# Optimization experiments

Hardware: AMD Instinct MI355X
Metric: run time of the kernel (lower is better)

Reference implementation:

```python
import jax, jax.numpy as jnp
import numpy as np

N_PEP = 50000
N_PROT = 50000
H = 256
F_IN = 1280
E = 300000
EL = 200000


def setup_inputs() -> dict:
    key = jax.random.key(0)
    ks = jax.random.split(key, 16)
    s = 0.02
    return {
        "x_pep": jax.random.normal(ks[0], (N_PEP, F_IN), jnp.float32),
        "x_prot": jax.random.normal(ks[1], (N_PROT, F_IN), jnp.float32),
        "Wpep": s * jax.random.normal(ks[2], (H, F_IN), jnp.float32),
        "bpep": jnp.zeros((H,), jnp.float32),
        "Wprot": s * jax.random.normal(ks[3], (H, F_IN), jnp.float32),
        "bprot": jnp.zeros((H,), jnp.float32),
        "Wl1": s * jax.random.normal(ks[4], (3, H, H), jnp.float32),
        "bl1": jnp.zeros((3, H), jnp.float32),
        "Wr1": s * jax.random.normal(ks[5], (3, H, H), jnp.float32),
        "Wl2": s * jax.random.normal(ks[6], (3, H, H), jnp.float32),
        "bl2": jnp.zeros((3, H), jnp.float32),
        "Wr2": s * jax.random.normal(ks[7], (3, H, H), jnp.float32),
        "ei_pp": jax.random.randint(ks[8], (2, E), 0, N_PEP, jnp.int32),   # pep -> prot
        "ei_rp": jax.random.randint(ks[9], (2, E), 0, N_PROT, jnp.int32),  # prot -> pep (reverse)
        "ei_prot": jax.random.randint(ks[10], (2, E), 0, N_PROT, jnp.int32),  # prot -> prot
        "eli_het": jax.random.randint(ks[11], (2, EL), 0, N_PEP, jnp.int32),
        "eli_homo": jax.random.randint(ks[12], (2, EL), 0, N_PROT, jnp.int32),
    }


def _seg_mean(src_feat, dst_idx, n_dst):
    # mean aggregation of edge messages into destination nodes
    s = jax.ops.segment_sum(src_feat, dst_idx, num_segments=n_dst)
    cnt = jax.ops.segment_sum(jnp.ones((dst_idx.shape[0], 1), src_feat.dtype), dst_idx, num_segments=n_dst)
    return s / jnp.maximum(cnt, 1.0)


def _sage(x_src, x_dst, ei, Wl, bl, Wr):
    # PyG SAGEConv(aggr='mean'): lin_l(mean_j x_j) + lin_r(x_i); lin_r has no bias
    m = _seg_mean(x_src[ei[0]], ei[1], x_dst.shape[0])
    return m @ Wl.T + bl + x_dst @ Wr.T


def reference(x_pep, x_prot, Wpep, bpep, Wprot, bprot,
              Wl1, bl1, Wr1, Wl2, bl2, Wr2,
              ei_pp, ei_rp, ei_prot, eli_het, eli_homo):
    # feat_src == 'esm': linear projection of ESM features
    h_pep = x_pep @ Wpep.T + bpep
    h_prot = x_prot @ Wprot.T + bprot

    # --- hetero SAGE layer 1 (to_hetero: sum over edge types per dst type) ---
    p1 = jax.nn.relu(_sage(h_prot, h_pep, ei_rp, Wl1[1], bl1[1], Wr1[1]))
    q1 = jax.nn.relu(_sage(h_pep, h_prot, ei_pp, Wl1[0], bl1[0], Wr1[0])
                     + _sage(h_prot, h_prot, ei_prot, Wl1[2], bl1[2], Wr1[2]))

    # --- hetero SAGE layer 2 ---
    p2 = _sage(q1, p1, ei_rp, Wl2[1], bl2[1], Wr2[1])
    q2 = (_sage(p1, q1, ei_pp, Wl2[0], bl2[0], Wr2[0])
          + _sage(q1, q1, ei_prot, Wl2[2], bl2[2], Wr2[2]))

    # edge classifiers: gather + elementwise mul + sum
    het_pred = (p2[eli_het[0]] * q2[eli_het[1]]).sum(axis=-1)
    homo_pred = (q2[eli_homo[0]] * q2[eli_homo[1]]).sum(axis=-1)
    return (het_pred, homo_pred)
```

## Files before the change

### kernel.cpp

```cpp
#include <hip/hip_runtime.h>

using u16 = unsigned short;
using u32 = unsigned int;

#define H 256
#define NNODE 50000
#define CAP 32
#define BM 128
#define BN 128
#define BK 64

typedef __attribute__((ext_vector_type(8))) short bf16x8;
typedef __attribute__((ext_vector_type(4))) float f32x4;

struct AChunks { const void* p[3]; };

__device__ __forceinline__ u16 f2b(float f) {
    u32 u = __builtin_bit_cast(u32, f);
    return (u16)((u + 0x7FFFu + ((u >> 16) & 1u)) >> 16);
}
__device__ __forceinline__ float b2f(u16 h) {
    u32 u = ((u32)h) << 16;
    return __builtin_bit_cast(float, u);
}
__device__ __forceinline__ void gld_lds16(const void* g, void* l) {
    __builtin_amdgcn_global_load_lds(
        (__attribute__((address_space(1))) void*)(void*)g,
        (__attribute__((address_space(3))) void*)l, 16, 0, 0);
}
__device__ __forceinline__ u32 packbf(float a, float b) {
    return (u32)f2b(a) | ((u32)f2b(b) << 16);
}

template<bool AF32, bool RELU>
__global__ __launch_bounds__(512) void gemm_pipe(
    AChunks ac, int aStride, const u16* __restrict__ Bw,
    const float* __restrict__ bias, u16* __restrict__ C, int M, int Ktot)
{
    __shared__ __align__(16) char As[2][BM * 128];
    __shared__ __align__(16) char Bs[2][BN * 128];

    const int tid = threadIdx.x;
    const int l   = tid & 63;
    const int w   = tid >> 6;
    const int wr  = w >> 2, wc = w & 3;
    const int m0  = blockIdx.x * BM;
    const int n0  = blockIdx.y * BN;
    const int nk  = Ktot >> 6;

    f32x4 acc[4][2];
#pragma unroll
    for (int i = 0; i < 4; ++i)
#pragma unroll
        for (int j = 0; j < 2; ++j) acc[i][j] = f32x4{0.f, 0.f, 0.f, 0.f};

    auto stageB = [&](int k, int bi) {
        int k0 = k * 64;
#pragma unroll
        for (int i = 0; i < 2; ++i) {
            int ci = i * 512 + tid;
            int r = ci >> 3, c16 = ci & 7;
            int sb = (c16 * 16) ^ ((r & 7) << 4);
            const u16* g = Bw + (size_t)(n0 + r) * Ktot + k0 + (sb >> 1);
            gld_lds16(g, &Bs[bi][ci * 16]);
        }
    };
    auto stageAb = [&](int k, int bi) {
        int k0 = k * 64;
        const u16* base = (const u16*)ac.p[k0 >> 8];
        int kk = k0 & 255;
#pragma unroll
        for (int i = 0; i < 2; ++i) {
            int ci = i * 512 + tid;
            int r = ci >> 3, c16 = ci & 7;
            int row = m0 + r; row = row < M ? row : M - 1;
            int sb = (c16 * 16) ^ ((r & 7) << 4);
            const u16* g = base + (size_t)row * aStride + kk + (sb >> 1);
            gld_lds16(g, &As[bi][ci * 16]);
        }
    };
    auto loadAf = [&](int k, float4 (&rA)[4]) {
        int k0 = k * 64;
        const float* base = (const float*)ac.p[0];
        int r = tid >> 2;
        int row = m0 + r; row = row < M ? row : M - 1;
        const float* g = base + (size_t)row * aStride + k0 + (tid & 3) * 16;
#pragma unroll
        for (int j = 0; j < 4; ++j) rA[j] = *(const float4*)(g + j * 4);
    };
    auto writeAf = [&](float4 (&rA)[4], int bi) {
        int r  = tid >> 2;
        int cb = (tid & 3) * 32;
        int sw = (r & 7) << 4;
        uint4 lo, hi;
        lo.x = packbf(rA[0].x, rA[0].y); lo.y = packbf(rA[0].z, rA[0].w);
        lo.z = packbf(rA[1].x, rA[1].y); lo.w = packbf(rA[1].z, rA[1].w);
        hi.x = packbf(rA[2].x, rA[2].y); hi.y = packbf(rA[2].z, rA[2].w);
        hi.z = packbf(rA[3].x, rA[3].y); hi.w = packbf(rA[3].z, rA[3].w);
        *(uint4*)&As[bi][r * 128 + (cb ^ sw)]        = lo;
        *(uint4*)&As[bi][r * 128 + ((cb + 16) ^ sw)] = hi;
    };
    auto compute = [&](int bi) {
#pragma unroll
        for (int ks = 0; ks < 2; ++ks) {
            bf16x8 af[4], bfr[2];
#pragma unroll
            for (int mi = 0; mi < 4; ++mi) {
                int r = wr * 64 + mi * 16 + (l & 15);
                int off = (ks * 64 + (l >> 4) * 16) ^ ((r & 7) << 4);
                af[mi] = *(const bf16x8*)&As[bi][r * 128 + off];
            }
#pragma unroll
            for (int ni = 0; ni < 2; ++ni) {
                int r = wc * 32 + ni * 16 + (l & 15);
                int off = (ks * 64 + (l >> 4) * 16) ^ ((r & 7) << 4);
                bfr[ni] = *(const bf16x8*)&Bs[bi][r * 128 + off];
            }
#pragma unroll
            for (int mi = 0; mi < 4; ++mi)
#pragma unroll
                for (int ni = 0; ni < 2; ++ni)
                    acc[mi][ni] = __builtin_amdgcn_mfma_f32_16x16x32_bf16(
                        af[mi], bfr[ni], acc[mi][ni], 0, 0, 0);
        }
    };
    auto body = [&](int k, float4 (&rA)[4], int cur) {
        if (AF32) {
            asm volatile("s_waitcnt vmcnt(6)" ::: "memory");
            writeAf(rA, cur);
            asm volatile("s_waitcnt lgkmcnt(0)" ::: "memory");
        } else {
            asm volatile("s_waitcnt vmcnt(4)" ::: "memory");
        }
        __builtin_amdgcn_sched_barrier(0);
        __builtin_amdgcn_s_barrier();
        __builtin_amdgcn_sched_barrier(0);
        compute(cur);
        __builtin_amdgcn_sched_barrier(0);
        __builtin_amdgcn_s_barrier();
        __builtin_amdgcn_sched_barrier(0);
        int kq = k + 2; if (kq > nk - 1) kq = nk - 1;
        stageB(kq, cur);
        __builtin_amdgcn_sched_barrier(0);
        if (AF32) loadAf(kq, rA);
        else      stageAb(kq, cur);
        __builtin_amdgcn_sched_barrier(0);
    };

    float4 rA0[4], rA1[4];
    if (AF32) {
        stageB(0, 0); __builtin_amdgcn_sched_barrier(0);
        loadAf(0, rA0); __builtin_amdgcn_sched_barrier(0);
        stageB(1, 1); __builtin_amdgcn_sched_barrier(0);
        loadAf(1, rA1); __builtin_amdgcn_sched_barrier(0);
    } else {
        stageB(0, 0); stageAb(0, 0);
        __builtin_amdgcn_sched_barrier(0);
        stageB(1, 1); stageAb(1, 1);
        __builtin_amdgcn_sched_barrier(0);
    }
    for (int k = 0; k < nk; k += 2) {
        body(k,     rA0, 0);
        body(k + 1, rA1, 1);
    }

    const int fr = l & 15, fq = l >> 4;
#pragma unroll
    for (int ni = 0; ni < 2; ++ni) {
        int col = n0 + wc * 32 + ni * 16 + fr;
        float bv = bias ? bias[col] : 0.f;
#pragma unroll
        for (int mi = 0; mi < 4; ++mi) {
            int rowb = m0 + wr * 64 + mi * 16 + fq * 4;
#pragma unroll
            for (int j = 0; j < 4; ++j) {
                int row = rowb + j;
                if (row < M) {
                    float v = acc[mi][ni][j] + bv;
                    if (RELU) v = fmaxf(v, 0.f);
                    C[(size_t)row * H + col] = f2b(v);
                }
            }
        }
    }
}

__global__ __launch_bounds__(256) void fill_zero(float4* __restrict__ p, size_t n4)
{
    size_t i = (size_t)blockIdx.x * blockDim.x + threadIdx.x;
    size_t stride = (size_t)gridDim.x * blockDim.x;
    for (; i < n4; i += stride) p[i] = make_float4(0.f, 0.f, 0.f, 0.f);
}

__global__ __launch_bounds__(256) void build_bucket(
    const int* __restrict__ src, const int* __restrict__ dst, int nE,
    int* __restrict__ cnt, int* __restrict__ bucket)
{
    int i = blockIdx.x * blockDim.x + threadIdx.x;
    if (i >= nE) return;
    int d = dst[i];
    int pos = atomicAdd(&cnt[d], 1);
    if (pos < CAP) bucket[(size_t)d * CAP + pos] = src[i];
}

__global__ __launch_bounds__(256) void seg_mean_gather(
    const u16* __restrict__ feat, const int* __restrict__ bucket,
    const int* __restrict__ cnt, int n_dst, u16* __restrict__ out)
{
    int d = (int)(((size_t)blockIdx.x * blockDim.x + threadIdx.x) >> 6);
    int lane = threadIdx.x & 63;
    if (d >= n_dst) return;
    int c = cnt[d];
    int cc = c < CAP ? c : CAP;
    const int* b = bucket + (size_t)d * CAP;
    float a0 = 0.f, a1 = 0.f, a2 = 0.f, a3 = 0.f;
    int i = 0;
    for (; i + 4 <= cc; i += 4) {
        int s0 = b[i], s1 = b[i + 1], s2 = b[i + 2], s3 = b[i + 3];
        uint2 v0 = *(const uint2*)(feat + (size_t)s0 * H + lane * 4);
        uint2 v1 = *(const uint2*)(feat + (size_t)s1 * H + lane * 4);
        uint2 v2 = *(const uint2*)(feat + (size_t)s2 * H + lane * 4);
        uint2 v3 = *(const uint2*)(feat + (size_t)s3 * H + lane * 4);
        a0 += b2f((u16)(v0.x & 0xffff)) + b2f((u16)(v1.x & 0xffff))
            + b2f((u16)(v2.x & 0xffff)) + b2f((u16)(v3.x & 0xffff));
        a1 += b2f((u16)(v0.x >> 16)) + b2f((u16)(v1.x >> 16))
            + b2f((u16)(v2.x >> 16)) + b2f((u16)(v3.x >> 16));
        a2 += b2f((u16)(v0.y & 0xffff)) + b2f((u16)(v1.y & 0xffff))
            + b2f((u16)(v2.y & 0xffff)) + b2f((u16)(v3.y & 0xffff));
        a3 += b2f((u16)(v0.y >> 16)) + b2f((u16)(v1.y >> 16))
            + b2f((u16)(v2.y >> 16)) + b2f((u16)(v3.y >> 16));
    }
    for (; i < cc; ++i) {
        uint2 v = *(const uint2*)(feat + (size_t)b[i] * H + lane * 4);
        a0 += b2f((u16)(v.x & 0xffff));
        a1 += b2f((u16)(v.x >> 16));
        a2 += b2f((u16)(v.y & 0xffff));
        a3 += b2f((u16)(v.y >> 16));
    }
    float inv = 1.0f / fmaxf((float)c, 1.0f);
    uint2 o;
    o.x = packbf(a0 * inv, a1 * inv);
    o.y = packbf(a2 * inv, a3 * inv);
    *(uint2*)(out + (size_t)d * H + lane * 4) = o;
}

__global__ __launch_bounds__(256) void edge_dot(
    const u16* __restrict__ P, const u16* __restrict__ Q,
    const int* __restrict__ ia, const int* __restrict__ ib,
    int nE, float* __restrict__ out)
{
    int gi = blockIdx.x * 256 + threadIdx.x;
    int e = gi >> 5, l32 = gi & 31;
    if (e >= nE) return;
    uint4 a = *(const uint4*)(P + (size_t)ia[e] * H + l32 * 8);
    uint4 b = *(const uint4*)(Q + (size_t)ib[e] * H + l32 * 8);
    float v = 0.f;
    v += b2f((u16)(a.x & 0xffff)) * b2f((u16)(b.x & 0xffff));
    v += b2f((u16)(a.x >> 16))    * b2f((u16)(b.x >> 16));
    v += b2f((u16)(a.y & 0xffff)) * b2f((u16)(b.y & 0xffff));
    v += b2f((u16)(a.y >> 16))    * b2f((u16)(b.y >> 16));
    v += b2f((u16)(a.z & 0xffff)) * b2f((u16)(b.z & 0xffff));
    v += b2f((u16)(a.z >> 16))    * b2f((u16)(b.z >> 16));
    v += b2f((u16)(a.w & 0xffff)) * b2f((u16)(b.w & 0xffff));
    v += b2f((u16)(a.w >> 16))    * b2f((u16)(b.w >> 16));
#pragma unroll
    for (int off = 16; off; off >>= 1) v += __shfl_xor(v, off);
    if (l32 == 0) out[e] = v;
}

struct PackTab {
    const float* s1[12]; const float* s2[12]; u16* dst[12];
    int Ks[12], Kdst[12], koff[12], blk0[13];
};
__global__ __launch_bounds__(256) void pack_all(PackTab t)
{
    int b = blockIdx.x;
    int it = 0;
    while (it < 11 && b >= t.blk0[it + 1]) ++it;
    int idx = (b - t.blk0[it]) * 1024 + threadIdx.x * 4;
    int Ks = t.Ks[it];
    if (idx >= 256 * Ks) return;
    int n = idx / Ks;
    int k = idx - n * Ks;
    float4 v = *(const float4*)(t.s1[it] + idx);
    if (t.s2[it]) {
        float4 u = *(const float4*)(t.s2[it] + idx);
        v.x += u.x; v.y += u.y; v.z += u.z; v.w += u.w;
    }
    ushort4 h;
    h.x = f2b(v.x); h.y = f2b(v.y); h.z = f2b(v.z); h.w = f2b(v.w);
    *(ushort4*)(t.dst[it] + (size_t)n * t.Kdst[it] + t.koff[it] + k) = h;
}

__global__ void bias_pair(const float* __restrict__ bl1, const float* __restrict__ bl2,
                          float* __restrict__ bq1, float* __restrict__ bq2)
{
    int i = threadIdx.x;
    if (blockIdx.x == 0) bq1[i] = bl1[i] + bl1[512 + i];
    else                 bq2[i] = bl2[i] + bl2[512 + i];
}

static inline void launch_gemm3(const void* a0, const void* a1, const void* a2,
                                const u16* Bw, const float* bias, u16* C,
                                int Ktot, bool relu, hipStream_t s)
{
    AChunks ac = {{a0, a1, a2}};
    dim3 grid((NNODE + BM - 1) / BM, H / BN);
    if (relu) gemm_pipe<false, true><<<grid, 512, 0, s>>>(ac, 256, Bw, bias, C, NNODE, Ktot);
    else      gemm_pipe<false, false><<<grid, 512, 0, s>>>(ac, 256, Bw, bias, C, NNODE, Ktot);
}

extern "C" void kernel_launch(void* const* d_in, const int* in_sizes, int n_in,
                              void* d_out, int out_size, void* d_ws, size_t ws_size,
                              hipStream_t stream)
{
    const float* x_pep  = (const float*)d_in[0];
    const float* x_prot = (const float*)d_in[1];
    const float* Wpep   = (const float*)d_in[2];
    const float* bpep   = (const float*)d_in[3];
    const float* Wprot  = (const float*)d_in[4];
    const float* bprot  = (const float*)d_in[5];
    const float* Wl1    = (const float*)d_in[6];
    const float* bl1    = (const float*)d_in[7];
    const float* Wr1    = (const float*)d_in[8];
    const float* Wl2    = (const float*)d_in[9];
    const float* bl2    = (const float*)d_in[10];
    const float* Wr2    = (const float*)d_in[11];
    const int* ei_pp    = (const int*)d_in[12];
    const int* ei_rp    = (const int*)d_in[13];
    const int* ei_prot  = (const int*)d_in[14];
    const int* eli_het  = (const int*)d_in[15];
    const int* eli_homo = (const int*)d_in[16];

    const int E  = in_sizes[12] / 2;
    const int EL = in_sizes[15] / 2;
    const int FIN = in_sizes[2] / H;

    float* out = (float*)d_out;

    const size_t nodeElems = (size_t)NNODE * H;
    u16* bufA = (u16*)d_ws;
    u16* bufB = bufA + nodeElems;
    u16* bufC = bufB + nodeElems;
    u16* bufD = bufC + nodeElems;
    u16* bufE = bufD + nodeElems;
    u16* bufF = bufE + nodeElems;
    u16* Bpep  = bufF + nodeElems;
    u16* Bprot = Bpep  + (size_t)256 * 1280;
    u16* Bp1   = Bprot + (size_t)256 * 1280;
    u16* Bq1   = Bp1   + (size_t)256 * 512;
    u16* Bp2   = Bq1   + (size_t)256 * 768;
    u16* Bq2   = Bp2   + (size_t)256 * 512;
    float* bq1 = (float*)(Bq2 + (size_t)256 * 768);
    float* bq2 = bq1 + 256;
    int* cntRP   = (int*)(bq2 + 256);
    int* cntPP   = cntRP + NNODE;
    int* cntPR   = cntPP + NNODE;
    int* bktRP   = cntPR + NNODE;
    int* bktPP   = bktRP + (size_t)NNODE * CAP;
    int* bktPR   = bktPP + (size_t)NNODE * CAP;

    const size_t HH = (size_t)H * H;

    PackTab t{};
    int blk = 0, it = 0;
    auto add = [&](const float* s1, const float* s2, u16* d, int Ks, int Kd, int ko) {
        t.s1[it] = s1; t.s2[it] = s2; t.dst[it] = d;
        t.Ks[it] = Ks; t.Kdst[it] = Kd; t.koff[it] = ko;
        t.blk0[it] = blk; blk += (256 * Ks) / 1024; ++it;
    };
    add(Wpep,  nullptr, Bpep,  1280, 1280, 0);
    add(Wprot, nullptr, Bprot, 1280, 1280, 0);
    add(Wl1 + 1 * HH, nullptr,      Bp1, 256, 512, 0);
    add(Wr1 + 1 * HH, nullptr,      Bp1, 256, 512, 256);
    add(Wl1 + 0 * HH, nullptr,      Bq1, 256, 768, 0);
    add(Wl1 + 2 * HH, nullptr,      Bq1, 256, 768, 256);
    add(Wr1 + 0 * HH, Wr1 + 2 * HH, Bq1, 256, 768, 512);
    add(Wl2 + 1 * HH, nullptr,      Bp2, 256, 512, 0);
    add(Wr2 + 1 * HH, nullptr,      Bp2, 256, 512, 256);
    add(Wl2 + 0 * HH, nullptr,      Bq2, 256, 768, 0);
    add(Wl2 + 2 * HH, nullptr,      Bq2, 256, 768, 256);
    add(Wr2 + 0 * HH, Wr2 + 2 * HH, Bq2, 256, 768, 512);
    t.blk0[12] = blk;
    pack_all<<<blk, 256, 0, stream>>>(t);
    bias_pair<<<2, 256, 0, stream>>>(bl1, bl2, bq1, bq2);

    fill_zero<<<147, 256, 0, stream>>>((float4*)cntRP, (size_t)3 * NNODE / 4);
    build_bucket<<<(E + 255) / 256, 256, 0, stream>>>(ei_rp,   ei_rp + E,   E, cntRP, bktRP);
    build_bucket<<<(E + 255) / 256, 256, 0, stream>>>(ei_pp,   ei_pp + E,   E, cntPP, bktPP);
    build_bucket<<<(E + 255) / 256, 256, 0, stream>>>(ei_prot, ei_prot + E, E, cntPR, bktPR);

    {
        dim3 grid((NNODE + BM - 1) / BM, H / BN);
        AChunks ap = {{x_pep, nullptr, nullptr}};
        gemm_pipe<true, false><<<grid, 512, 0, stream>>>(ap, FIN, Bpep, bpep, bufA, NNODE, FIN);
        AChunks aq = {{x_prot, nullptr, nullptr}};
        gemm_pipe<true, false><<<grid, 512, 0, stream>>>(aq, FIN, Bprot, bprot, bufB, NNODE, FIN);
    }

    const int gG = (NNODE * 64 + 255) / 256;
    seg_mean_gather<<<gG, 256, 0, stream>>>(bufB, bktRP, cntRP, NNODE, bufE);
    launch_gemm3(bufE, bufA, nullptr, Bp1, bl1 + 256, bufC, 512, true, stream);
    seg_mean_gather<<<gG, 256, 0, stream>>>(bufA, bktPP, cntPP, NNODE, bufE);
    seg_mean_gather<<<gG, 256, 0, stream>>>(bufB, bktPR, cntPR, NNODE, bufF);
    launch_gemm3(bufE, bufF, bufB, Bq1, bq1, bufD, 768, true, stream);

    seg_mean_gather<<<gG, 256, 0, stream>>>(bufD, bktRP, cntRP, NNODE, bufE);
    launch_gemm3(bufE, bufC, nullptr, Bp2, bl2 + 256, bufA, 512, false, stream);
    seg_mean_gather<<<gG, 256, 0, stream>>>(bufC, bktPP, cntPP, NNODE, bufE);
    seg_mean_gather<<<gG, 256, 0, stream>>>(bufD, bktPR, cntPR, NNODE, bufF);
    launch_gemm3(bufE, bufF, bufD, Bq2, bq2, bufB, 768, false, stream);

    edge_dot<<<(EL * 32 + 255) / 256, 256, 0, stream>>>(bufA, bufB, eli_het,  eli_het  + EL, EL, out);
    edge_dot<<<(EL * 32 + 255) / 256, 256, 0, stream>>>(bufB, bufB, eli_homo, eli_homo + EL, EL, out + EL);
}
```

Before: 699.3 us.

## Add dedicated fp32-input projection GEMM with full-N tile and async LDS loads

Replaces the fp32-A path of the generic GEMM with a dedicated projection kernel. Each block computes all 256 output columns, so the large fp32 activation matrix is read once instead of twice across two N-blocks. fp32 A tiles are loaded straight into LDS with global_load_lds and converted to bf16 by truncation when fragments are read, instead of a register-staged round-to-nearest conversion. The risks are slight precision loss from truncation and more accumulator registers per thread, which may lower occupancy.

```diff
diff --git a/kernel.cpp b/kernel.cpp
--- a/kernel.cpp
+++ b/kernel.cpp
@@ -12,6 +12,7 @@
 
 typedef __attribute__((ext_vector_type(8))) short bf16x8;
 typedef __attribute__((ext_vector_type(4))) float f32x4;
+typedef __attribute__((ext_vector_type(4))) unsigned int u32x4;
 
 struct AChunks { const void* p[3]; };
 
@@ -31,8 +32,12 @@
 __device__ __forceinline__ u32 packbf(float a, float b) {
     return (u32)f2b(a) | ((u32)f2b(b) << 16);
 }
-
-template<bool AF32, bool RELU>
+__device__ __forceinline__ u32 pack_trunc(float lo, float hi) {
+    return __builtin_amdgcn_perm(__builtin_bit_cast(u32, hi),
+                                 __builtin_bit_cast(u32, lo), 0x07060302u);
+}
+
+template<bool RELU>
 __global__ __launch_bounds__(512) void gemm_pipe(
     AChunks ac, int aStride, const u16* __restrict__ Bw,
     const float* __restrict__ bias, u16* __restrict__ C, int M, int Ktot)
@@ -79,27 +84,6 @@
             gld_lds16(g, &As[bi][ci * 16]);
         }
     };
-    auto loadAf = [&](int k, float4 (&rA)[4]) {
-        int k0 = k * 64;
-        const float* base = (const float*)ac.p[0];
-        int r = tid >> 2;
-        int row = m0 + r; row = row < M ? row : M - 1;
-        const float* g = base + (size_t)row * aStride + k0 + (tid & 3) * 16;
-#pragma unroll
-        for (int j = 0; j < 4; ++j) rA[j] = *(const float4*)(g + j * 4);
-    };
-    auto writeAf = [&](float4 (&rA)[4], int bi) {
-        int r  = tid >> 2;
-        int cb = (tid & 3) * 32;
-        int sw = (r & 7) << 4;
-        uint4 lo, hi;
-        lo.x = packbf(rA[0].x, rA[0].y); lo.y = packbf(rA[0].z, rA[0].w);
-        lo.z = packbf(rA[1].x, rA[1].y); lo.w = packbf(rA[1].z, rA[1].w);
-        hi.x = packbf(rA[2].x, rA[2].y); hi.y = packbf(rA[2].z, rA[2].w);
-        hi.z = packbf(rA[3].x, rA[3].y); hi.w = packbf(rA[3].z, rA[3].w);
-        *(uint4*)&As[bi][r * 128 + (cb ^ sw)]        = lo;
-        *(uint4*)&As[bi][r * 128 + ((cb + 16) ^ sw)] = hi;
-    };
     auto compute = [&](int bi) {
 #pragma unroll
         for (int ks = 0; ks < 2; ++ks) {
@@ -124,14 +108,8 @@
                         af[mi], bfr[ni], acc[mi][ni], 0, 0, 0);
         }
     };
-    auto body = [&](int k, float4 (&rA)[4], int cur) {
-        if (AF32) {
-            asm volatile("s_waitcnt vmcnt(6)" ::: "memory");
-            writeAf(rA, cur);
-            asm volatile("s_waitcnt lgkmcnt(0)" ::: "memory");
-        } else {
-            asm volatile("s_waitcnt vmcnt(4)" ::: "memory");
-        }
+    auto body = [&](int k, int cur) {
+        asm volatile("s_waitcnt vmcnt(4)" ::: "memory");
         __builtin_amdgcn_sched_barrier(0);
         __builtin_amdgcn_s_barrier();
         __builtin_amdgcn_sched_barrier(0);
@@ -141,27 +119,17 @@
         __builtin_amdgcn_sched_barrier(0);
         int kq = k + 2; if (kq > nk - 1) kq = nk - 1;
         stageB(kq, cur);
-        __builtin_amdgcn_sched_barrier(0);
-        if (AF32) loadAf(kq, rA);
-        else      stageAb(kq, cur);
-        __builtin_amdgcn_sched_barrier(0);
-    };
-
-    float4 rA0[4], rA1[4];
-    if (AF32) {
-        stageB(0, 0); __builtin_amdgcn_sched_barrier(0);
-        loadAf(0, rA0); __builtin_amdgcn_sched_barrier(0);
-        stageB(1, 1); __builtin_amdgcn_sched_barrier(0);
-        loadAf(1, rA1); __builtin_amdgcn_sched_barrier(0);
-    } else {
-        stageB(0, 0); stageAb(0, 0);
-        __builtin_amdgcn_sched_barrier(0);
-        stageB(1, 1); stageAb(1, 1);
-        __builtin_amdgcn_sched_barrier(0);
-    }
+        stageAb(kq, cur);
+        __builtin_amdgcn_sched_barrier(0);
+    };
+
+    stageB(0, 0); stageAb(0, 0);
+    __builtin_amdgcn_sched_barrier(0);
+    stageB(1, 1); stageAb(1, 1);
+    __builtin_amdgcn_sched_barrier(0);
     for (int k = 0; k < nk; k += 2) {
-        body(k,     rA0, 0);
-        body(k + 1, rA1, 1);
+        body(k,     0);
+        body(k + 1, 1);
     }
 
     const int fr = l & 15, fq = l >> 4;
@@ -180,6 +148,120 @@
                     if (RELU) v = fmaxf(v, 0.f);
                     C[(size_t)row * H + col] = f2b(v);
                 }
+            }
+        }
+    }
+}
+
+__global__ __launch_bounds__(512) void gemm_proj(
+    const float* __restrict__ A, int aStride, const u16* __restrict__ Bw,
+    const float* __restrict__ bias, u16* __restrict__ C, int M, int Ktot)
+{
+    __shared__ __align__(16) char As[2][128 * 128];
+    __shared__ __align__(16) char Bs[2][256 * 64];
+
+    const int tid = threadIdx.x;
+    const int l   = tid & 63;
+    const int w   = tid >> 6;
+    const int wr  = w >> 2, wc = w & 3;
+    const int m0  = blockIdx.x * 128;
+    const int nk  = Ktot >> 5;
+
+    f32x4 acc[4][4];
+#pragma unroll
+    for (int i = 0; i < 4; ++i)
+#pragma unroll
+        for (int j = 0; j < 4; ++j) acc[i][j] = f32x4{0.f, 0.f, 0.f, 0.f};
+
+    auto stageB = [&](int k, int bi) {
+        int k0 = k * 32;
+#pragma unroll
+        for (int i = 0; i < 2; ++i) {
+            int ci = i * 512 + tid;
+            int r = ci >> 2, c4 = ci & 3;
+            int sb = (c4 * 16) ^ ((r & 3) << 4);
+            const u16* g = Bw + (size_t)r * Ktot + k0 + (sb >> 1);
+            gld_lds16(g, &Bs[bi][ci * 16]);
+        }
+    };
+    auto stageA = [&](int k, int bi) {
+        int k0 = k * 32;
+#pragma unroll
+        for (int i = 0; i < 2; ++i) {
+            int ci = i * 512 + tid;
+            int r = ci >> 3, c8 = ci & 7;
+            int row = m0 + r; row = row < M ? row : M - 1;
+            int sb = (c8 * 16) ^ ((r & 7) << 4);
+            const float* g = A + (size_t)row * aStride + k0 + (sb >> 2);
+            gld_lds16(g, &As[bi][ci * 16]);
+        }
+    };
+    auto compute = [&](int bi) {
+        bf16x8 af[4], bfr[4];
+#pragma unroll
+        for (int mi = 0; mi < 4; ++mi) {
+            int r = wr * 64 + mi * 16 + (l & 15);
+            int o0 = ((l >> 4) * 32)      ^ ((r & 7) << 4);
+            int o1 = ((l >> 4) * 32 + 16) ^ ((r & 7) << 4);
+            f32x4 c0 = *(const f32x4*)&As[bi][r * 128 + o0];
+            f32x4 c1 = *(const f32x4*)&As[bi][r * 128 + o1];
+            u32x4 ww;
+            ww[0] = pack_trunc(c0[0], c0[1]);
+            ww[1] = pack_trunc(c0[2], c0[3]);
+            ww[2] = pack_trunc(c1[0], c1[1]);
+            ww[3] = pack_trunc(c1[2], c1[3]);
+            af[mi] = __builtin_bit_cast(bf16x8, ww);
+        }
+#pragma unroll
+        for (int ni = 0; ni < 4; ++ni) {
+            int r = wc * 64 + ni * 16 + (l & 15);
+            int off = ((l >> 4) * 16) ^ ((r & 3) << 4);
+            bfr[ni] = *(const bf16x8*)&Bs[bi][r * 64 + off];
+        }
+#pragma unroll
+        for (int mi = 0; mi < 4; ++mi)
+#pragma unroll
+            for (int ni = 0; ni < 4; ++ni)
+                acc[mi][ni] = __builtin_amdgcn_mfma_f32_16x16x32_bf16(
+                    af[mi], bfr[ni], acc[mi][ni], 0, 0, 0);
+    };
+    auto body = [&](int k, int cur) {
+        asm volatile("s_waitcnt vmcnt(4)" ::: "memory");
+        __builtin_amdgcn_sched_barrier(0);
+        __builtin_amdgcn_s_barrier();
+        __builtin_amdgcn_sched_barrier(0);
+        compute(cur);
+        __builtin_amdgcn_sched_barrier(0);
+        __builtin_amdgcn_s_barrier();
+        __builtin_amdgcn_sched_barrier(0);
+        int kq = k + 2; if (kq > nk - 1) kq = nk - 1;
+        stageB(kq, cur);
+        stageA(kq, cur);
+        __builtin_amdgcn_sched_barrier(0);
+    };
+
+    stageB(0, 0); stageA(0, 0);
+    __builtin_amdgcn_sched_barrier(0);
+    stageB(1, 1); stageA(1, 1);
+    __builtin_amdgcn_sched_barrier(0);
+    for (int k = 0; k < nk; k += 2) {
+        body(k,     0);
+        body(k + 1, 1);
+    }
+
+    const int fr = l & 15, fq = l >> 4;
+#pragma unroll
+    for (int ni = 0; ni < 4; ++ni) {
+        int col = wc * 64 + ni * 16 + fr;
+        float bv = bias ? bias[col] : 0.f;
+#pragma unroll
+        for (int mi = 0; mi < 4; ++mi) {
+            int rowb = m0 + wr * 64 + mi * 16 + fq * 4;
+#pragma unroll
+            for (int j = 0; j < 4; ++j) {
+                int row = rowb + j;
+                if (row < M)
+                    C[(size_t)row * H + col] = f2b(acc[mi][ni][j] + bv);
             }
         }
     }
@@ -306,8 +388,8 @@
 {
     AChunks ac = {{a0, a1, a2}};
     dim3 grid((NNODE + BM - 1) / BM, H / BN);
-    if (relu) gemm_pipe<false, true><<<grid, 512, 0, s>>>(ac, 256, Bw, bias, C, NNODE, Ktot);
-    else      gemm_pipe<false, false><<<grid, 512, 0, s>>>(ac, 256, Bw, bias, C, NNODE, Ktot);
+    if (relu) gemm_pipe<true><<<grid, 512, 0, s>>>(ac, 256, Bw, bias, C, NNODE, Ktot);
+    else      gemm_pipe<false><<<grid, 512, 0, s>>>(ac, 256, Bw, bias, C, NNODE, Ktot);
 }
 
 extern "C" void kernel_launch(void* const* d_in, const int* in_sizes, int n_in,
@@ -391,11 +473,9 @@
     build_bucket<<<(E + 255) / 256, 256, 0, stream>>>(ei_prot, ei_prot + E, E, cntPR, bktPR);
 
     {
-        dim3 grid((NNODE + BM - 1) / BM, H / BN);
-        AChunks ap = {{x_pep, nullptr, nullptr}};
-        gemm_pipe<true, false><<<grid, 512, 0, stream>>>(ap, FIN, Bpep, bpep, bufA, NNODE, FIN);
-        AChunks aq = {{x_prot, nullptr, nullptr}};
-        gemm_pipe<true, false><<<grid, 512, 0, stream>>>(aq, FIN, Bprot, bprot, bufB, NNODE, FIN);
+        dim3 grid((NNODE + 127) / 128, 1);
+        gemm_proj<<<grid, 512, 0, stream>>>(x_pep,  FIN, Bpep,  bpep,  bufA, NNODE, FIN);
+        gemm_proj<<<grid, 512, 0, stream>>>(x_prot, FIN, Bprot, bprot, bufB, NNODE, FIN);
     }
 
     const int gG = (NNODE * 64 + 255) / 256;
```

New measurement: 660.2 us. 1.06x faster.
